# Kernel optimization log

Measured on AMD Instinct MI355X. Metric: run time of the kernel, lower is better.

Reference implementation:

```python
import jax, jax.numpy as jnp
import numpy as np

N_NODES = 100000

def _sage_conv(h, src, dst, Wl, bl, Wr):
    # PyG SAGEConv (mean aggr): out = lin_l(mean_{j in N(i)} h_j) + lin_r(h_i)
    msg = h[src]                                            # [E, H] gather
    agg = jax.ops.segment_sum(msg, dst, num_segments=N_NODES)   # [N, H] scatter-add
    cnt = jax.ops.segment_sum(jnp.ones((src.shape[0],), h.dtype), dst, num_segments=N_NODES)
    mean = agg / jnp.maximum(cnt, 1.0)[:, None]
    return mean @ Wl + bl + h @ Wr

def setup_inputs() -> dict:
    key = jax.random.key(0)
    ks = jax.random.split(key, 12)
    IN, H, C, E = 256, 128, 40, 1600000
    s = 0.05
    return {
        "x": jax.random.normal(ks[0], (N_NODES, IN), jnp.float32),
        "edge_index": jax.random.randint(ks[1], (2, E), 0, N_NODES, jnp.int32),
        "W_pre": jax.random.normal(ks[2], (IN, H), jnp.float32) * s,
        "b_pre": jnp.zeros((H,), jnp.float32),
        "Wl0": jax.random.normal(ks[3], (H, H), jnp.float32) * s,
        "bl0": jnp.zeros((H,), jnp.float32),
        "Wr0": jax.random.normal(ks[4], (H, H), jnp.float32) * s,
        "Wl1": jax.random.normal(ks[5], (H, H), jnp.float32) * s,
        "bl1": jnp.zeros((H,), jnp.float32),
        "Wr1": jax.random.normal(ks[6], (H, H), jnp.float32) * s,
        "W_post": jax.random.normal(ks[7], (H, C), jnp.float32) * s,
        "b_post": jnp.zeros((C,), jnp.float32),
    }

def reference(x, edge_index, W_pre, b_pre, Wl0, bl0, Wr0, Wl1, bl1, Wr1, W_post, b_post):
    src, dst = edge_index[0], edge_index[1]
    h = x @ W_pre + b_pre                       # pre Linear
    # two SAGEConv layers + relu (dropout is identity in eval mode)
    h = jax.nn.relu(_sage_conv(h, src, dst, Wl0, bl0, Wr0))
    h = jax.nn.relu(_sage_conv(h, src, dst, Wl1, bl1, Wr1))
    logits = h @ W_post + b_post                # post Linear
    return jax.nn.log_softmax(logits, axis=1)
```

## Files before the change

kernel.cpp:

```cpp
#include <hip/hip_runtime.h>
#include <hip/hip_bf16.h>
#include <math.h>

#define N_NODES 100000
#define IN_F 256
#define HID 128
#define NCLS 40

#define NB 782
#define BN 128
#define NC 448
#define CSZ2 3584

typedef __attribute__((ext_vector_type(8))) short short8;
typedef __attribute__((ext_vector_type(4))) float f32x4;

__device__ __forceinline__ short f2bf(float f){
  union { float f; unsigned u; } x; x.f = f;
  unsigned r = (x.u + 0x7fffu + ((x.u >> 16) & 1u)) >> 16;
  return (short)r;
}
__device__ __forceinline__ float bf2f(unsigned short u){
  union { unsigned u; float f; } x; x.u = ((unsigned)u) << 16;
  return x.f;
}

__global__ __launch_bounds__(256) void k_wprep(
    const float* __restrict__ Wpre, const float* __restrict__ Wl0,
    const float* __restrict__ Wr0,  const float* __restrict__ Wl1,
    const float* __restrict__ Wr1,  const float* __restrict__ Wpost,
    unsigned short* __restrict__ img)
{
  const int g = blockIdx.x*256 + threadIdx.x;
  if(g >= 13056) return;
  const int base = g*8;
  unsigned short v[8];
  if(base < 98304){
    const int which = base >> 15;
    const int idx = base & 32767;
    const int l = (idx >> 3) & 63, kb = (idx >> 9) & 7, ct = idx >> 12;
    const int col = ct*16 + (l & 15);
    const float* Wsrc; int kbase;
    if(which == 0){ Wsrc = Wpre; kbase = kb*32 + (l>>4)*8; }
    else{
      Wsrc = (which==1) ? ((kb<4) ? Wl0 : Wr0) : ((kb<4) ? Wl1 : Wr1);
      kbase = (kb&3)*32 + (l>>4)*8;
    }
    #pragma unroll
    for(int j = 0; j < 8; j++) v[j] = (unsigned short)f2bf(Wsrc[(size_t)(kbase+j)*HID + col]);
  } else {
    const int idx = base - 98304;
    const int l = (idx >> 3) & 63, kb = (idx >> 9) & 3, ct = idx >> 11;
    const int col = ct*16 + (l & 15);
    const int kbase = kb*32 + (l>>4)*8;
    #pragma unroll
    for(int j = 0; j < 8; j++)
      v[j] = (col < NCLS) ? (unsigned short)f2bf(Wpost[(size_t)(kbase+j)*NCLS + col]) : 0;
  }
  *reinterpret_cast<short8*>(img + base) = *reinterpret_cast<const short8*>(v);
}

__global__ __launch_bounds__(256) void k_hist(const int* __restrict__ dst, int E,
                                              int* __restrict__ cnt){
  __shared__ int hist[NB];
  const int c = blockIdx.x;
  for(int i = threadIdx.x; i < NB; i += 256) hist[i] = 0;
  __syncthreads();
  const int s0 = c*CSZ2, s1 = min(s0 + CSZ2, E);
  for(int i = s0 + threadIdx.x; i < s1; i += 256)
    atomicAdd(&hist[(unsigned)__builtin_nontemporal_load(dst + i) >> 7], 1);
  __syncthreads();
  for(int i = threadIdx.x; i < NB; i += 256) cnt[c*NB + i] = hist[i];
}

__global__ __launch_bounds__(256) void k_bscanA(const int* __restrict__ cnt,
                                                int* __restrict__ wbase,
                                                int* __restrict__ btot){
  __shared__ int s[256];
  const int b = blockIdx.x;
  const int t = threadIdx.x;
  int v0 = 0, v1 = 0;
  if(2*t < NC)     v0 = cnt[(2*t)*NB + b];
  if(2*t + 1 < NC) v1 = cnt[(2*t+1)*NB + b];
  s[t] = v0 + v1; __syncthreads();
  for(int d = 1; d < 256; d <<= 1){
    int add = (t >= d) ? s[t-d] : 0;
    __syncthreads();
    s[t] += add;
    __syncthreads();
  }
  const int ex = (t > 0) ? s[t-1] : 0;
  if(2*t < NC)     wbase[(2*t)*NB + b] = ex;
  if(2*t + 1 < NC) wbase[(2*t+1)*NB + b] = ex + v0;
  if(t == 255) btot[b] = s[255];
}

__global__ __launch_bounds__(1024) void k_bscanB(const int* __restrict__ btot,
                                                 int* __restrict__ bstart, int E){
  __shared__ int s[1024];
  const int t = threadIdx.x;
  int v = (t < NB) ? btot[t] : 0;
  s[t] = v; __syncthreads();
  for(int d = 1; d < 1024; d <<= 1){
    int add = (t >= d) ? s[t-d] : 0;
    __syncthreads();
    s[t] += add;
    __syncthreads();
  }
  if(t < NB) bstart[t] = s[t] - v;
  if(t == 0) bstart[NB] = E;
}

__global__ __launch_bounds__(256) void k_place(const int* __restrict__ src,
                                               const int* __restrict__ dst, int E,
                                               const int* __restrict__ wbase,
                                               const int* __restrict__ bstart,
                                               int* __restrict__ pk){
  const int g = blockIdx.x;
  const int c = (g & 7)*(NC/8) + (g >> 3);
  __shared__ int cur[NB];
  for(int i = threadIdx.x; i < NB; i += 256)
    cur[i] = wbase[c*NB + i] + bstart[i];
  __syncthreads();
  const int s0 = c*CSZ2, s1 = min(s0 + CSZ2, E);
  for(int i = s0 + threadIdx.x; i < s1; i += 256){
    const int d  = __builtin_nontemporal_load(dst + i);
    const int sv = __builtin_nontemporal_load(src + i);
    const int pos = atomicAdd(&cur[(unsigned)d >> 7], 1);
    pk[pos] = ((d & 127) << 17) | sv;
  }
}

__global__ __launch_bounds__(512) void k_sortb(const int* __restrict__ pk,
                                               const int* __restrict__ bstart,
                                               int* __restrict__ esrc2,
                                               int* __restrict__ nodeoff, int E){
  __shared__ int hist[BN];
  __shared__ int nofs[BN];
  __shared__ int curs[BN];
  const int b = blockIdx.x;
  const int t = threadIdx.x;
  const int bs = bstart[b];
  const int ne = bstart[b+1] - bs;
  for(int i = t; i < BN; i += 512) hist[i] = 0;
  __syncthreads();
  for(int i = t; i < ne; i += 512)
    atomicAdd(&hist[(unsigned)pk[bs + i] >> 17], 1);
  __syncthreads();
  if(t < BN) nofs[t] = hist[t];
  __syncthreads();
  for(int d = 1; d < BN; d <<= 1){
    int add = 0;
    if(t < BN && t >= d) add = nofs[t-d];
    __syncthreads();
    if(t < BN) nofs[t] += add;
    __syncthreads();
  }
  if(t < BN){
    curs[t] = nofs[t] - hist[t];
    const int node = b*BN + t;
    if(node < N_NODES) nodeoff[node] = bs + nofs[t] - hist[t];
    if(node == N_NODES - 1 || (b == NB-1 && t == BN-1)) nodeoff[N_NODES] = E;
  }
  __syncthreads();
  for(int i = t; i < ne; i += 512){
    const int e = pk[bs + i];
    const int pos = atomicAdd(&curs[(unsigned)e >> 17], 1);
    esrc2[bs + pos] = e & 0x1ffff;
  }
}

__global__ __launch_bounds__(256) void k_agg3(
    const unsigned short* __restrict__ h, const int* __restrict__ nodeoff,
    const int* __restrict__ esrc2, unsigned short* __restrict__ mean)
{
  const int lane = threadIdx.x & 63;
  const int wid = blockIdx.x*4 + (threadIdx.x >> 6);
  const int wstride = gridDim.x*4;
  const unsigned* hp = (const unsigned*)h;
  for(int node = wid; node < N_NODES; node += wstride){
    const int beg = nodeoff[node];
    const int deg = nodeoff[node+1] - beg;
    float a0 = 0.f, a1 = 0.f;
    for(int base = 0; base < deg; base += 64){
      const int rem = deg - base;
      const int cnt = rem < 64 ? rem : 64;
      const int myi = (lane < cnt) ? esrc2[beg + base + lane] : 0;
      int e = 0;
      for(; e + 8 <= cnt; e += 8){
        unsigned v[8];
        #pragma unroll
        for(int u = 0; u < 8; u++){
          const int s = __builtin_amdgcn_readlane(myi, e + u);
          v[u] = hp[(size_t)s*64 + lane];
        }
        #pragma unroll
        for(int u = 0; u < 8; u++){
          a0 += bf2f((unsigned short)(v[u] & 0xffffu));
          a1 += bf2f((unsigned short)(v[u] >> 16));
        }
      }
      for(; e < cnt; e++){
        const int s = __builtin_amdgcn_readlane(myi, e);
        const unsigned vv = hp[(size_t)s*64 + lane];
        a0 += bf2f((unsigned short)(vv & 0xffffu));
        a1 += bf2f((unsigned short)(vv >> 16));
      }
    }
    const float inv = (deg > 0) ? (1.0f/(float)deg) : 0.f;
    a0 *= inv; a1 *= inv;
    const unsigned o = ((unsigned)(unsigned short)f2bf(a1) << 16) | (unsigned)(unsigned short)f2bf(a0);
    ((unsigned*)mean)[(size_t)node*64 + lane] = o;
  }
}

__global__ __launch_bounds__(256) void k_gemm_pre(
    const float* __restrict__ x, const unsigned short* __restrict__ wimg,
    const float* __restrict__ b, unsigned short* __restrict__ out)
{
  __shared__ short wlds[8*8*64*8];
  const int t = threadIdx.x;
  {
    short8* dstp = reinterpret_cast<short8*>(wlds);
    const short8* srcp = reinterpret_cast<const short8*>(wimg);
    #pragma unroll
    for(int i = 0; i < 16; i++) dstp[t + i*256] = srcp[t + i*256];
  }
  __syncthreads();
  const int wave = t >> 6, lane = t & 63;
  const int r_in = lane & 15, kg = lane >> 4;
  const int NT = N_NODES/16, stride = gridDim.x*4;

  auto loadx = [&](int tile, float4 (&xa)[8], float4 (&xb)[8]){
    const float* xp = x + (size_t)(tile*16 + r_in)*IN_F + kg*8;
    #pragma unroll
    for(int kb = 0; kb < 8; kb++){
      xa[kb] = *reinterpret_cast<const float4*>(xp + kb*32);
      xb[kb] = *reinterpret_cast<const float4*>(xp + kb*32 + 4);
    }
  };
  auto compute = [&](int tile, const float4 (&xa)[8], const float4 (&xb)[8]){
    f32x4 acc[8];
    #pragma unroll
    for(int ct = 0; ct < 8; ct++) acc[ct] = (f32x4){0.f,0.f,0.f,0.f};
    #pragma unroll
    for(int kb = 0; kb < 8; kb++){
      short8 a;
      a[0]=f2bf(xa[kb].x); a[1]=f2bf(xa[kb].y); a[2]=f2bf(xa[kb].z); a[3]=f2bf(xa[kb].w);
      a[4]=f2bf(xb[kb].x); a[5]=f2bf(xb[kb].y); a[6]=f2bf(xb[kb].z); a[7]=f2bf(xb[kb].w);
      #pragma unroll
      for(int ct = 0; ct < 8; ct++){
        short8 bb = *reinterpret_cast<const short8*>(&wlds[((ct*8+kb)*64+lane)*8]);
        acc[ct] = __builtin_amdgcn_mfma_f32_16x16x32_bf16(a, bb, acc[ct], 0, 0, 0);
      }
    }
    const int row0 = tile*16;
    #pragma unroll
    for(int ct = 0; ct < 8; ct++){
      const int col = ct*16 + r_in;
      const float bias = b[col];
      #pragma unroll
      for(int i = 0; i < 4; i++)
        out[(size_t)(row0 + kg*4 + i)*HID + col] = (unsigned short)f2bf(acc[ct][i] + bias);
    }
  };

  int tile = blockIdx.x*4 + wave;
  if(tile >= NT) return;
  float4 xaA[8], xbA[8], xaB[8], xbB[8];
  loadx(tile, xaA, xbA);
  for(;;){
    int nt = tile + stride;
    bool more = nt < NT;
    if(more) loadx(nt, xaB, xbB);
    compute(tile, xaA, xbA);
    if(!more) break;
    tile = nt;
    nt = tile + stride;
    more = nt < NT;
    if(more) loadx(nt, xaA, xbA);
    compute(tile, xaB, xbB);
    if(!more) break;
    tile = nt;
  }
}

__global__ __launch_bounds__(256) void k_gemm_sage(
    const unsigned short* __restrict__ mean, const unsigned short* __restrict__ h,
    const unsigned short* __restrict__ wimg, const float* __restrict__ bl,
    unsigned short* __restrict__ out)
{
  __shared__ short wlds[8*8*64*8];
  const int t = threadIdx.x;
  {
    short8* dstp = reinterpret_cast<short8*>(wlds);
    const short8* srcp = reinterpret_cast<const short8*>(wimg);
    #pragma unroll
    for(int i = 0; i < 16; i++) dstp[t + i*256] = srcp[t + i*256];
  }
  __syncthreads();
  const int wave = t >> 6, lane = t & 63;
  const int r_in = lane & 15, kg = lane >> 4;
  for(int tile = blockIdx.x*4 + wave; tile < N_NODES/16; tile += gridDim.x*4){
    const int row0 = tile*16;
    f32x4 acc[8];
    #pragma unroll
    for(int ct = 0; ct < 8; ct++) acc[ct] = (f32x4){0.f,0.f,0.f,0.f};
    #pragma unroll
    for(int kb = 0; kb < 8; kb++){
      const unsigned short* in = (kb < 4) ? mean : h;
      const int koff = (kb & 3)*32 + kg*8;
      short8 a = *reinterpret_cast<const short8*>(in + (size_t)(row0 + r_in)*HID + koff);
      #pragma unroll
      for(int ct = 0; ct < 8; ct++){
        short8 bb = *reinterpret_cast<const short8*>(&wlds[((ct*8+kb)*64+lane)*8]);
        acc[ct] = __builtin_amdgcn_mfma_f32_16x16x32_bf16(a, bb, acc[ct], 0, 0, 0);
      }
    }
    #pragma unroll
    for(int ct = 0; ct < 8; ct++){
      const int col = ct*16 + r_in;
      const float bias = bl[col];
      #pragma unroll
      for(int i = 0; i < 4; i++){
        const int row = row0 + kg*4 + i;
        float v = fmaxf(acc[ct][i] + bias, 0.f);
        out[(size_t)row*HID + col] = (unsigned short)f2bf(v);
      }
    }
  }
}

__global__ __launch_bounds__(256) void k_post(
    const unsigned short* __restrict__ h, const unsigned short* __restrict__ wimg,
    const float* __restrict__ b, float* __restrict__ out)
{
  __shared__ short wlds[3*4*64*8];
  __shared__ float bias_s[48];
  const int t = threadIdx.x;
  {
    short8* dstp = reinterpret_cast<short8*>(wlds);
    const short8* srcp = reinterpret_cast<const short8*>(wimg);
    for(int i = t; i < 768; i += 256) dstp[i] = srcp[i];
  }
  if(t < 48) bias_s[t] = (t < NCLS) ? b[t] : -1e30f;
  __syncthreads();
  const int wave = t >> 6, lane = t & 63;
  const int r_in = lane & 15, kg = lane >> 4;
  for(int tile = blockIdx.x*4 + wave; tile < N_NODES/16; tile += gridDim.x*4){
    const int row0 = tile*16;
    f32x4 acc[3];
    #pragma unroll
    for(int ct = 0; ct < 3; ct++) acc[ct] = (f32x4){0.f,0.f,0.f,0.f};
    #pragma unroll
    for(int kb = 0; kb < 4; kb++){
      short8 a = *reinterpret_cast<const short8*>(h + (size_t)(row0 + r_in)*HID + kb*32 + kg*8);
      #pragma unroll
      for(int ct = 0; ct < 3; ct++){
        short8 bb = *reinterpret_cast<const short8*>(&wlds[((ct*4+kb)*64+lane)*8]);
        acc[ct] = __builtin_amdgcn_mfma_f32_16x16x32_bf16(a, bb, acc[ct], 0, 0, 0);
      }
    }
    #pragma unroll
    for(int i = 0; i < 4; i++){
      float v0 = acc[0][i] + bias_s[r_in];
      float v1 = acc[1][i] + bias_s[16 + r_in];
      float v2 = acc[2][i] + bias_s[32 + r_in];
      float m = fmaxf(fmaxf(v0, v1), v2);
      #pragma unroll
      for(int o = 8; o > 0; o >>= 1) m = fmaxf(m, __shfl_xor(m, o));
      float s = expf(v0 - m) + expf(v1 - m) + expf(v2 - m);
      #pragma unroll
      for(int o = 8; o > 0; o >>= 1) s += __shfl_xor(s, o);
      const float ls = m + logf(s);
      const int row = row0 + kg*4 + i;
      float* op = out + (size_t)row*NCLS;
      op[r_in] = v0 - ls;
      op[16 + r_in] = v1 - ls;
      if(r_in < 8) op[32 + r_in] = v2 - ls;
    }
  }
}

extern "C" void kernel_launch(void* const* d_in, const int* in_sizes, int n_in,
                              void* d_out, int out_size, void* d_ws, size_t ws_size,
                              hipStream_t stream)
{
  const float* x      = (const float*)d_in[0];
  const int*   ei     = (const int*)  d_in[1];
  const float* W_pre  = (const float*)d_in[2];
  const float* b_pre  = (const float*)d_in[3];
  const float* Wl0    = (const float*)d_in[4];
  const float* bl0    = (const float*)d_in[5];
  const float* Wr0    = (const float*)d_in[6];
  const float* Wl1    = (const float*)d_in[7];
  const float* bl1    = (const float*)d_in[8];
  const float* Wr1    = (const float*)d_in[9];
  const float* W_post = (const float*)d_in[10];
  const float* b_post = (const float*)d_in[11];
  float* out = (float*)d_out;

  const int E = in_sizes[1] / 2;
  const int* src = ei;
  const int* dst = ei + E;

  char* ws = (char*)d_ws;
  size_t off = 0;
  auto alloc = [&](size_t bytes)->void*{
    void* p = ws + off;
    off += (bytes + 255) & ~(size_t)255;
    return p;
  };
  unsigned short* hA = (unsigned short*)alloc((size_t)N_NODES*HID*2);
  unsigned short* hB = (unsigned short*)alloc((size_t)N_NODES*HID*2);
  unsigned short* hM = (unsigned short*)alloc((size_t)N_NODES*HID*2);
  int* pk      = (int*)alloc((size_t)E*4);
  int* esrc2   = (int*)alloc((size_t)E*4);
  int* cnt     = (int*)alloc((size_t)NC*NB*4);
  int* wbase   = (int*)alloc((size_t)NC*NB*4);
  int* btot    = (int*)alloc((size_t)NB*4);
  int* bstart  = (int*)alloc((size_t)(NB+1)*4);
  int* nodeoff = (int*)alloc((size_t)(N_NODES+1)*4);
  unsigned short* wimg = (unsigned short*)alloc(104448*2);

  k_wprep<<<51, 256, 0, stream>>>(W_pre, Wl0, Wr0, Wl1, Wr1, W_post, wimg);

  k_hist<<<NC, 256, 0, stream>>>(dst, E, cnt);
  k_bscanA<<<NB, 256, 0, stream>>>(cnt, wbase, btot);
  k_bscanB<<<1, 1024, 0, stream>>>(btot, bstart, E);
  k_place<<<NC, 256, 0, stream>>>(src, dst, E, wbase, bstart, pk);
  k_sortb<<<NB, 512, 0, stream>>>(pk, bstart, esrc2, nodeoff, E);

  k_gemm_pre<<<512, 256, 0, stream>>>(x, wimg, b_pre, hA);

  k_agg3<<<4096, 256, 0, stream>>>(hA, nodeoff, esrc2, hM);
  k_gemm_sage<<<1563, 256, 0, stream>>>(hM, hA, wimg + 32768, bl0, hB);

  k_agg3<<<4096, 256, 0, stream>>>(hB, nodeoff, esrc2, hM);
  k_gemm_sage<<<1563, 256, 0, stream>>>(hM, hB, wimg + 65536, bl1, hA);

  k_post<<<1563, 256, 0, stream>>>(hA, wimg + 98304, b_post, out);
}
```

Before: 278.7 us.

## Fuse neighbor mean aggregation with SAGE GEMM via LDS-staged tile

Merges the gather/mean aggregation kernel and the SAGEConv GEMM into one kernel. Each wave aggregates 16 nodes into a swizzled LDS buffer, then runs MFMA on that tile together with the self features. This removes the global round-trip of the mean matrix and one launch per layer. In exchange the grid drops from 4096 to 512 blocks and every block now holds the 64KB weight image in LDS, which lowers occupancy and the latency hiding available to the irregular gather.

```diff
diff --git a/kernel.cpp b/kernel.cpp
--- a/kernel.cpp
+++ b/kernel.cpp
@@ -170,47 +170,93 @@
   }
 }
 
-__global__ __launch_bounds__(256) void k_agg3(
+__global__ __launch_bounds__(256) void k_agg_sage(
     const unsigned short* __restrict__ h, const int* __restrict__ nodeoff,
-    const int* __restrict__ esrc2, unsigned short* __restrict__ mean)
+    const int* __restrict__ esrc2, const unsigned short* __restrict__ wimg,
+    const float* __restrict__ bl, unsigned short* __restrict__ out)
 {
-  const int lane = threadIdx.x & 63;
-  const int wid = blockIdx.x*4 + (threadIdx.x >> 6);
-  const int wstride = gridDim.x*4;
+  __shared__ short wlds[8*8*64*8];
+  __shared__ unsigned mean_lds[4][16][64];
+  const int t = threadIdx.x;
+  {
+    short8* dstp = reinterpret_cast<short8*>(wlds);
+    const short8* srcp = reinterpret_cast<const short8*>(wimg);
+    #pragma unroll
+    for(int i = 0; i < 16; i++) dstp[t + i*256] = srcp[t + i*256];
+  }
+  __syncthreads();
+  const int wave = t >> 6, lane = t & 63;
+  const int r_in = lane & 15, kg = lane >> 4;
   const unsigned* hp = (const unsigned*)h;
-  for(int node = wid; node < N_NODES; node += wstride){
-    const int beg = nodeoff[node];
-    const int deg = nodeoff[node+1] - beg;
-    float a0 = 0.f, a1 = 0.f;
-    for(int base = 0; base < deg; base += 64){
-      const int rem = deg - base;
-      const int cnt = rem < 64 ? rem : 64;
-      const int myi = (lane < cnt) ? esrc2[beg + base + lane] : 0;
-      int e = 0;
-      for(; e + 8 <= cnt; e += 8){
-        unsigned v[8];
-        #pragma unroll
-        for(int u = 0; u < 8; u++){
-          const int s = __builtin_amdgcn_readlane(myi, e + u);
-          v[u] = hp[(size_t)s*64 + lane];
+  float bias_r[8];
+  #pragma unroll
+  for(int ct = 0; ct < 8; ct++) bias_r[ct] = bl[ct*16 + r_in];
+
+  for(int tile = blockIdx.x*4 + wave; tile < N_NODES/16; tile += gridDim.x*4){
+    const int row0 = tile*16;
+    for(int n = 0; n < 16; n++){
+      const int node = row0 + n;
+      const int beg = nodeoff[node];
+      const int deg = nodeoff[node+1] - beg;
+      float a0 = 0.f, a1 = 0.f;
+      for(int base = 0; base < deg; base += 64){
+        const int rem = deg - base;
+        const int cnt = rem < 64 ? rem : 64;
+        const int myi = (lane < cnt) ? esrc2[beg + base + lane] : 0;
+        int e = 0;
+        for(; e + 8 <= cnt; e += 8){
+          unsigned v[8];
+          #pragma unroll
+          for(int u = 0; u < 8; u++)
+            v[u] = hp[(size_t)__builtin_amdgcn_readlane(myi, e + u)*64 + lane];
+          #pragma unroll
+          for(int u = 0; u < 8; u++){
+            a0 += bf2f((unsigned short)(v[u] & 0xffffu));
+            a1 += bf2f((unsigned short)(v[u] >> 16));
+          }
         }
-        #pragma unroll
-        for(int u = 0; u < 8; u++){
-          a0 += bf2f((unsigned short)(v[u] & 0xffffu));
-          a1 += bf2f((unsigned short)(v[u] >> 16));
+        for(; e < cnt; e++){
+          const unsigned vv = hp[(size_t)__builtin_amdgcn_readlane(myi, e)*64 + lane];
+          a0 += bf2f((unsigned short)(vv & 0xffffu));
+          a1 += bf2f((unsigned short)(vv >> 16));
         }
       }
-      for(; e < cnt; e++){
-        const int s = __builtin_amdgcn_readlane(myi, e);
-        const unsigned vv = hp[(size_t)s*64 + lane];
-        a0 += bf2f((unsigned short)(vv & 0xffffu));
-        a1 += bf2f((unsigned short)(vv >> 16));
+      const float inv = (deg > 0) ? (1.0f/(float)deg) : 0.f;
+      const unsigned o = ((unsigned)(unsigned short)f2bf(a1*inv) << 16)
+                       |  (unsigned)(unsigned short)f2bf(a0*inv);
+      mean_lds[wave][n][lane ^ (n << 2)] = o;
+    }
+    asm volatile("s_waitcnt lgkmcnt(0)" ::: "memory");
+    __builtin_amdgcn_sched_barrier(0);
+
+    short8 am[4], ah[4];
+    #pragma unroll
+    for(int kb = 0; kb < 4; kb++){
+      const int cbase = (kb*16 + kg*4) ^ (r_in << 2);
+      am[kb] = *reinterpret_cast<const short8*>(&mean_lds[wave][r_in][cbase]);
+      ah[kb] = *reinterpret_cast<const short8*>(h + (size_t)(row0 + r_in)*HID + kb*32 + kg*8);
+    }
+    f32x4 acc[8];
+    #pragma unroll
+    for(int ct = 0; ct < 8; ct++) acc[ct] = (f32x4){0.f,0.f,0.f,0.f};
+    #pragma unroll
+    for(int kb = 0; kb < 8; kb++){
+      short8 a = (kb < 4) ? am[kb & 3] : ah[kb & 3];
+      #pragma unroll
+      for(int ct = 0; ct < 8; ct++){
+        short8 bb = *reinterpret_cast<const short8*>(&wlds[((ct*8+kb)*64+lane)*8]);
+        acc[ct] = __builtin_amdgcn_mfma_f32_16x16x32_bf16(a, bb, acc[ct], 0, 0, 0);
       }
     }
-    const float inv = (deg > 0) ? (1.0f/(float)deg) : 0.f;
-    a0 *= inv; a1 *= inv;
-    const unsigned o = ((unsigned)(unsigned short)f2bf(a1) << 16) | (unsigned)(unsigned short)f2bf(a0);
-    ((unsigned*)mean)[(size_t)node*64 + lane] = o;
+    #pragma unroll
+    for(int ct = 0; ct < 8; ct++){
+      const int col = ct*16 + r_in;
+      #pragma unroll
+      for(int i = 0; i < 4; i++){
+        float v = fmaxf(acc[ct][i] + bias_r[ct], 0.f);
+        out[(size_t)(row0 + kg*4 + i)*HID + col] = (unsigned short)f2bf(v);
+      }
+    }
   }
 }
 
@@ -285,52 +331,6 @@
   }
 }
 
-__global__ __launch_bounds__(256) void k_gemm_sage(
-    const unsigned short* __restrict__ mean, const unsigned short* __restrict__ h,
-    const unsigned short* __restrict__ wimg, const float* __restrict__ bl,
-    unsigned short* __restrict__ out)
-{
-  __shared__ short wlds[8*8*64*8];
-  const int t = threadIdx.x;
-  {
-    short8* dstp = reinterpret_cast<short8*>(wlds);
-    const short8* srcp = reinterpret_cast<const short8*>(wimg);
-    #pragma unroll
-    for(int i = 0; i < 16; i++) dstp[t + i*256] = srcp[t + i*256];
-  }
-  __syncthreads();
-  const int wave = t >> 6, lane = t & 63;
-  const int r_in = lane & 15, kg = lane >> 4;
-  for(int tile = blockIdx.x*4 + wave; tile < N_NODES/16; tile += gridDim.x*4){
-    const int row0 = tile*16;
-    f32x4 acc[8];
-    #pragma unroll
-    for(int ct = 0; ct < 8; ct++) acc[ct] = (f32x4){0.f,0.f,0.f,0.f};
-    #pragma unroll
-    for(int kb = 0; kb < 8; kb++){
-      const unsigned short* in = (kb < 4) ? mean : h;
-      const int koff = (kb & 3)*32 + kg*8;
-      short8 a = *reinterpret_cast<const short8*>(in + (size_t)(row0 + r_in)*HID + koff);
-      #pragma unroll
-      for(int ct = 0; ct < 8; ct++){
-        short8 bb = *reinterpret_cast<const short8*>(&wlds[((ct*8+kb)*64+lane)*8]);
-        acc[ct] = __builtin_amdgcn_mfma_f32_16x16x32_bf16(a, bb, acc[ct], 0, 0, 0);
-      }
-    }
-    #pragma unroll
-    for(int ct = 0; ct < 8; ct++){
-      const int col = ct*16 + r_in;
-      const float bias = bl[col];
-      #pragma unroll
-      for(int i = 0; i < 4; i++){
-        const int row = row0 + kg*4 + i;
-        float v = fmaxf(acc[ct][i] + bias, 0.f);
-        out[(size_t)row*HID + col] = (unsigned short)f2bf(v);
-      }
-    }
-  }
-}
-
 __global__ __launch_bounds__(256) void k_post(
     const unsigned short* __restrict__ h, const unsigned short* __restrict__ wimg,
     const float* __restrict__ b, float* __restrict__ out)
@@ -413,7 +413,6 @@
   };
   unsigned short* hA = (unsigned short*)alloc((size_t)N_NODES*HID*2);
   unsigned short* hB = (unsigned short*)alloc((size_t)N_NODES*HID*2);
-  unsigned short* hM = (unsigned short*)alloc((size_t)N_NODES*HID*2);
   int* pk      = (int*)alloc((size_t)E*4);
   int* esrc2   = (int*)alloc((size_t)E*4);
   int* cnt     = (int*)alloc((size_t)NC*NB*4);
@@ -433,11 +432,9 @@
 
   k_gemm_pre<<<512, 256, 0, stream>>>(x, wimg, b_pre, hA);
 
-  k_agg3<<<4096, 256, 0, stream>>>(hA, nodeoff, esrc2, hM);
-  k_gemm_sage<<<1563, 256, 0, stream>>>(hM, hA, wimg + 32768, bl0, hB);
-
-  k_agg3<<<4096, 256, 0, stream>>>(hB, nodeoff, esrc2, hM);
-  k_gemm_sage<<<1563, 256, 0, stream>>>(hM, hB, wimg + 65536, bl1, hA);
+  k_agg_sage<<<512, 256, 0, stream>>>(hA, nodeoff, esrc2, wimg + 32768, bl0, hB);
+
+  k_agg_sage<<<512, 256, 0, stream>>>(hB, nodeoff, esrc2, wimg + 65536, bl1, hA);
 
   k_post<<<1563, 256, 0, stream>>>(hA, wimg + 98304, b_post, out);
 }
```

Result: slower. 442.6 us (+58.8%).
